# Kernel optimization log

Hardware: AMD Instinct MI355X
Metric: run time of the kernel (lower is better)

## Reference

```python
import jax, jax.numpy as jnp
import numpy as np

B, T, N_EMBD, N_HEAD = 2, 2048, 1024, 16
HEAD = N_EMBD // N_HEAD
WINDOW = 64


def setup_inputs() -> dict:
    key = jax.random.key(0)
    kq, kk, kv, kw = jax.random.split(key, 4)
    q = jax.random.normal(kq, (B, T, N_EMBD), dtype=jnp.float32)
    k = jax.random.normal(kk, (B, T, N_EMBD), dtype=jnp.float32)
    v = jax.random.normal(kv, (B, T, N_EMBD), dtype=jnp.float32)
    W_proj = jax.random.normal(kw, (N_EMBD, N_EMBD), dtype=jnp.float32) * (1.0 / np.sqrt(N_EMBD))
    b_proj = jnp.zeros((N_EMBD,), dtype=jnp.float32)
    return {"q": q, "k": k, "v": v, "W_proj": W_proj, "b_proj": b_proj}


def reference(q, k, v, W_proj, b_proj):
    Bsz, Tlen, _ = q.shape
    # split heads: [B, H, T, D]
    qh = q.reshape(Bsz, Tlen, N_HEAD, HEAD).transpose(0, 2, 1, 3)
    kh = k.reshape(Bsz, Tlen, N_HEAD, HEAD).transpose(0, 2, 1, 3)
    vh = v.reshape(Bsz, Tlen, N_HEAD, HEAD).transpose(0, 2, 1, 3)

    scale = 1.0 / np.sqrt(HEAD)
    scores = jnp.einsum('bhqd,bhkd->bhqk', qh, kh) * scale  # [B,H,T,T]

    # windowed additive mask: positions with |i-j| > WINDOW get -inf
    idx = jnp.arange(Tlen)
    dist = jnp.abs(idx[None, :] - idx[:, None])  # [T, T]
    scores = jnp.where(dist[None, None] > WINDOW, -jnp.inf, scores)

    attn = jax.nn.softmax(scores, axis=-1)
    y = jnp.einsum('bhqk,bhkd->bhqd', attn, vh)  # [B,H,T,D]
    y = y.transpose(0, 2, 1, 3).reshape(Bsz, Tlen, N_EMBD)
    return y @ W_proj.T + b_proj
```

## Files before the change

kernel.cpp:

```cpp
#include <hip/hip_runtime.h>
#include <hip/hip_bf16.h>

#define B_SZ 2
#define T_SZ 2048
#define NE   1024
#define NH   16
#define HD   64
#define WIN  64
#define QT   64
#define KT   192
#define GM   4096
#define GN   1024
#define GK   1024
#define KPAD 72
#define VPAD 200

__device__ ushort Wb_static[GN * GK];

__device__ __forceinline__ uint pack2(float lo, float hi) {
    uint r;
    asm("v_cvt_pk_bf16_f32 %0, %1, %2" : "=v"(r) : "v"(lo), "v"(hi));
    return r;
}
__device__ __forceinline__ uint4 pack8(float4 a, float4 b) {
    return make_uint4(pack2(a.x, a.y), pack2(a.z, a.w),
                      pack2(b.x, b.y), pack2(b.z, b.w));
}

typedef __attribute__((ext_vector_type(8))) short frag_ab;
typedef __attribute__((ext_vector_type(4))) float frag_cd;
union FragU { frag_ab f; uint u[4]; };

#define LDS_BAR() do {                                        \
    asm volatile("s_waitcnt lgkmcnt(0)" ::: "memory");        \
    __builtin_amdgcn_s_barrier();                             \
    asm volatile("" ::: "memory");                            \
} while (0)

#define VM_BAR(N) do {                                        \
    asm volatile("s_waitcnt vmcnt(" #N ")" ::: "memory");     \
    __builtin_amdgcn_s_barrier();                             \
    asm volatile("" ::: "memory");                            \
} while (0)

__global__ __launch_bounds__(256, 3) void attn_mfma_kernel(
    const float* __restrict__ q, const float* __restrict__ k,
    const float* __restrict__ v, const float* __restrict__ W,
    ushort* __restrict__ y)
{
    __shared__ __attribute__((aligned(16))) ushort pool[KT * KPAD + HD * VPAD];
    ushort* Ks = pool;
    ushort* Vt = pool + KT * KPAD;
    ushort* Ps = pool;

    const int bid = blockIdx.x;
    const int swz = ((bid & 7) << 7) | (bid >> 3);
    const int qs  = (swz & 31) * QT;
    const int h   = (swz >> 5) & 15;
    const int b   = swz >> 9;
    const int t   = threadIdx.x;
    const int kstart = qs - WIN;

    const int wv   = t >> 6;
    const int L    = t & 63;
    const int r16  = L & 15;
    const int quad = L >> 4;

    float4 qf0, qf1, qg0, qg1;
    {
        const float* qrow = q + ((size_t)(b * T_SZ + qs + wv * 16 + r16)) * NE + h * HD;
        const float4* p0 = (const float4*)(qrow + quad * 8);
        const float4* p1 = (const float4*)(qrow + 32 + quad * 8);
        qf0 = p0[0]; qf1 = p0[1]; qg0 = p1[0]; qg1 = p1[1];
    }

    {
        const int idx = bid * 256 + t;
        const float4 f = ((const float4*)W)[idx];
        ((uint2*)Wb_static)[idx] = make_uint2(pack2(f.x, f.y), pack2(f.z, f.w));
    }

    float4 va[6], vb[6];
#pragma unroll
    for (int i = 0; i < 6; ++i) {
        const int c  = t + 256 * i;
        const int j  = c >> 3;
        const int cc = c & 7;
        const int d8 = cc * 8;
        const int jg = kstart + j;
        const int jc = min(max(jg, 0), T_SZ - 1);
        const size_t off = ((size_t)(b * T_SZ + jc)) * NE + h * HD + d8;
        const float4* kp = (const float4*)(k + off);
        const float4* vp = (const float4*)(v + off);
        va[i] = vp[0]; vb[i] = vp[1];
        const float4 k0 = kp[0], k1 = kp[1];
        *(uint4*)&Ks[j * KPAD + d8] = pack8(k0, k1);
    }

    const float QSC = 0.125f * 1.44269504f;
    frag_ab aq0, aq1;
    {
        FragU u0, u1;
        u0.u[0] = pack2(qf0.x * QSC, qf0.y * QSC);
        u0.u[1] = pack2(qf0.z * QSC, qf0.w * QSC);
        u0.u[2] = pack2(qf1.x * QSC, qf1.y * QSC);
        u0.u[3] = pack2(qf1.z * QSC, qf1.w * QSC);
        u1.u[0] = pack2(qg0.x * QSC, qg0.y * QSC);
        u1.u[1] = pack2(qg0.z * QSC, qg0.w * QSC);
        u1.u[2] = pack2(qg1.x * QSC, qg1.y * QSC);
        u1.u[3] = pack2(qg1.z * QSC, qg1.w * QSC);
        aq0 = u0.f; aq1 = u1.f;
    }
    LDS_BAR();

    frag_cd sacc[9];
#pragma unroll
    for (int i = 0; i < 9; ++i) sacc[i] = (frag_cd){0,0,0,0};
    __builtin_amdgcn_s_setprio(1);
#pragma unroll
    for (int i = 0; i < 9; ++i) {
        const int nb = wv + i;
        const frag_ab b0 = *(const frag_ab*)&Ks[(nb * 16 + r16) * KPAD + quad * 8];
        const frag_ab b1 = *(const frag_ab*)&Ks[(nb * 16 + r16) * KPAD + 32 + quad * 8];
        sacc[i] = __builtin_amdgcn_mfma_f32_16x16x32_bf16(aq0, b0, sacc[i], 0, 0, 0);
        sacc[i] = __builtin_amdgcn_mfma_f32_16x16x32_bf16(aq1, b1, sacc[i], 0, 0, 0);
    }
    __builtin_amdgcn_s_setprio(0);

    const int base_m = wv * 16 + quad * 4;
    float l[4] = {0.f, 0.f, 0.f, 0.f};
#pragma unroll
    for (int i = 0; i < 9; ++i) {
        const int jl = (wv + i) * 16 + r16;
        const int jg = kstart + jl;
        const bool jg_ok = (jg >= 0) & (jg < T_SZ);
#pragma unroll
        for (int r = 0; r < 4; ++r) {
            const int mrow = base_m + r;
            const bool valid = jg_ok & ((uint)(jl - mrow) <= 2u * WIN);
            const float p = valid ? exp2f(sacc[i][r]) : 0.0f;
            l[r] += p;
            sacc[i][r] = p;
        }
    }
#pragma unroll
    for (int r = 0; r < 4; ++r) {
        l[r] += __shfl_xor(l[r], 1);
        l[r] += __shfl_xor(l[r], 2);
        l[r] += __shfl_xor(l[r], 4);
        l[r] += __shfl_xor(l[r], 8);
    }

#pragma unroll
    for (int i = 0; i < 6; ++i) {
        const int c  = t + 256 * i;
        const int j  = c >> 3;
        const int cc = c & 7;
        const int d8 = cc * 8;
        ushort* vtc = &Vt[d8 * VPAD + (((j >> 3) ^ cc) * 8 + (j & 7))];
        const uint p01 = pack2(va[i].x, va[i].y);
        const uint p23 = pack2(va[i].z, va[i].w);
        const uint p45 = pack2(vb[i].x, vb[i].y);
        const uint p67 = pack2(vb[i].z, vb[i].w);
        vtc[0 * VPAD] = (ushort)p01; vtc[1 * VPAD] = (ushort)(p01 >> 16);
        vtc[2 * VPAD] = (ushort)p23; vtc[3 * VPAD] = (ushort)(p23 >> 16);
        vtc[4 * VPAD] = (ushort)p45; vtc[5 * VPAD] = (ushort)(p45 >> 16);
        vtc[6 * VPAD] = (ushort)p67; vtc[7 * VPAD] = (ushort)(p67 >> 16);
    }

    LDS_BAR();
#pragma unroll
    for (int i = 0; i < 9; ++i) {
        const int jl = (wv + i) * 16 + r16;
        const uint p01 = pack2(sacc[i][0], sacc[i][1]);
        const uint p23 = pack2(sacc[i][2], sacc[i][3]);
        Ps[(base_m + 0) * VPAD + jl] = (ushort)p01;
        Ps[(base_m + 1) * VPAD + jl] = (ushort)(p01 >> 16);
        Ps[(base_m + 2) * VPAD + jl] = (ushort)p23;
        Ps[(base_m + 3) * VPAD + jl] = (ushort)(p23 >> 16);
    }
    {
        const int zb = (wv & 1) ? (wv - 1) : (wv + 9);
        const int jl = zb * 16 + r16;
#pragma unroll
        for (int r = 0; r < 4; ++r)
            Ps[(base_m + r) * VPAD + jl] = 0;
    }
    LDS_BAR();

    const int kb0 = wv >> 1;
    frag_ab ap[5];
#pragma unroll
    for (int i = 0; i < 5; ++i)
        ap[i] = *(const frag_ab*)&Ps[(wv * 16 + r16) * VPAD + (kb0 + i) * 32 + quad * 8];

    frag_cd oacc[4];
#pragma unroll
    for (int nb = 0; nb < 4; ++nb) oacc[nb] = (frag_cd){0,0,0,0};
    __builtin_amdgcn_s_setprio(1);
#pragma unroll
    for (int nb = 0; nb < 4; ++nb) {
        const int dr  = nb * 16 + r16;
        const int dsw = (dr >> 3) & 7;
#pragma unroll
        for (int i = 0; i < 5; ++i) {
            const int kb = kb0 + i;
            const frag_ab bv = *(const frag_ab*)&Vt[dr * VPAD + (((kb * 4 + quad) ^ dsw) * 8)];
            oacc[nb] = __builtin_amdgcn_mfma_f32_16x16x32_bf16(ap[i], bv, oacc[nb], 0, 0, 0);
        }
    }
    __builtin_amdgcn_s_setprio(0);

    float inv[4];
#pragma unroll
    for (int r = 0; r < 4; ++r) inv[r] = 1.0f / l[r];
#pragma unroll
    for (int nb = 0; nb < 4; ++nb) {
        const int d  = nb * 16 + r16;
        const uint p01 = pack2(oacc[nb][0] * inv[0], oacc[nb][1] * inv[1]);
        const uint p23 = pack2(oacc[nb][2] * inv[2], oacc[nb][3] * inv[3]);
        const size_t rb = (size_t)(b * T_SZ + qs + base_m) * NE + h * HD + d;
        y[rb + 0 * NE] = (ushort)p01;
        y[rb + 1 * NE] = (ushort)(p01 >> 16);
        y[rb + 2 * NE] = (ushort)p23;
        y[rb + 3 * NE] = (ushort)(p23 >> 16);
    }
}

#define ASZ (128 * 64)
#define BSZ (64 * 64)

__global__ __launch_bounds__(256, 2) void proj_gemm_kernel(
    const ushort* __restrict__ A,
    const float* __restrict__ bias, float* __restrict__ C)
{
    __shared__ __attribute__((aligned(16))) ushort As[2 * ASZ];
    __shared__ __attribute__((aligned(16))) ushort Bs[2 * BSZ];

    const ushort* Bw = Wb_static;
    const int t   = threadIdx.x;
    const int bid = blockIdx.x;
    const int swz = ((bid & 7) << 6) | (bid >> 3);
    const int tile_n = swz & 15;
    const int tile_m = swz >> 4;
    const int lane   = t & 63;
    const int wv     = t >> 6;
    const int wm     = wv >> 1;
    const int wn     = wv & 1;
    const int r16    = lane & 15;
    const int quad   = lane >> 4;

    frag_cd acc[4][2];
#pragma unroll
    for (int mi = 0; mi < 4; ++mi)
#pragma unroll
        for (int ni = 0; ni < 2; ++ni)
            acc[mi][ni] = (frag_cd){0.0f, 0.0f, 0.0f, 0.0f};

    const int fm = wm * 64 + r16;
    const int fn = wn * 32 + r16;
    const int sw = r16 & 7;

#define STAGE_AB(buf, kk)                                                      \
    {                                                                          \
        _Pragma("unroll")                                                      \
        for (int i = 0; i < 4; ++i) {                                          \
            const int c   = t + 256 * i;                                       \
            const int row = c >> 3;                                            \
            const int src = ((c & 7) ^ (row & 7)) * 8;                         \
            __builtin_amdgcn_global_load_lds(                                  \
                (const __attribute__((address_space(1))) unsigned int*)        \
                    (A + (size_t)(tile_m * 128 + row) * GK + (kk) + src),      \
                (__attribute__((address_space(3))) unsigned int*)              \
                    (As + (buf) * ASZ + c * 8), 16, 0, 0);                     \
        }                                                                      \
        _Pragma("unroll")                                                      \
        for (int i = 0; i < 2; ++i) {                                          \
            const int c   = t + 256 * i;                                       \
            const int row = c >> 3;                                            \
            const int src = ((c & 7) ^ (row & 7)) * 8;                         \
            __builtin_amdgcn_global_load_lds(                                  \
                (const __attribute__((address_space(1))) unsigned int*)        \
                    (Bw + (size_t)(tile_n * 64 + row) * GK + (kk) + src),      \
                (__attribute__((address_space(3))) unsigned int*)              \
                    (Bs + (buf) * BSZ + c * 8), 16, 0, 0);                     \
        }                                                                      \
    }

#define COMPUTE_AB(buf)                                                        \
    {                                                                          \
        _Pragma("unroll")                                                      \
        for (int ks = 0; ks < 2; ++ks) {                                       \
            const int cidx = (((ks * 4) + quad) ^ sw) * 8;                     \
            frag_ab af[4], bfr[2];                                             \
            _Pragma("unroll")                                                  \
            for (int mi = 0; mi < 4; ++mi)                                     \
                af[mi] = *(const frag_ab*)                                     \
                    &As[(buf) * ASZ + (fm + mi * 16) * 64 + cidx];             \
            _Pragma("unroll")                                                  \
            for (int ni = 0; ni < 2; ++ni)                                     \
                bfr[ni] = *(const frag_ab*)                                    \
                    &Bs[(buf) * BSZ + (fn + ni * 16) * 64 + cidx];             \
            _Pragma("unroll")                                                  \
            for (int mi = 0; mi < 4; ++mi)                                     \
                _Pragma("unroll")                                              \
                for (int ni = 0; ni < 2; ++ni)                                 \
                    acc[mi][ni] = __builtin_amdgcn_mfma_f32_16x16x32_bf16(     \
                        af[mi], bfr[ni], acc[mi][ni], 0, 0, 0);                \
        }                                                                      \
    }

    STAGE_AB(0, 0);
    int cur = 0;
    for (int k0 = 0; k0 < GK - 64; k0 += 64) {
        STAGE_AB(cur ^ 1, k0 + 64);
        VM_BAR(6);
        COMPUTE_AB(cur);
        LDS_BAR();
        cur ^= 1;
    }
    {
        asm volatile("s_waitcnt vmcnt(0)" ::: "memory");
        __builtin_amdgcn_s_barrier();
        asm volatile("" ::: "memory");
        COMPUTE_AB(cur);
    }

#pragma unroll
    for (int mi = 0; mi < 4; ++mi) {
#pragma unroll
        for (int ni = 0; ni < 2; ++ni) {
            const int rbase = tile_m * 128 + wm * 64 + mi * 16 + quad * 4;
            const int cg    = tile_n * 64 + wn * 32 + ni * 16 + r16;
            const float bv  = bias[cg];
#pragma unroll
            for (int r = 0; r < 4; ++r)
                C[(size_t)(rbase + r) * GN + cg] = acc[mi][ni][r] + bv;
        }
    }
}

extern "C" void kernel_launch(void* const* d_in, const int* in_sizes, int n_in,
                              void* d_out, int out_size, void* d_ws, size_t ws_size,
                              hipStream_t stream) {
    (void)in_sizes; (void)n_in; (void)out_size; (void)ws_size;
    const float* q    = (const float*)d_in[0];
    const float* k    = (const float*)d_in[1];
    const float* v    = (const float*)d_in[2];
    const float* W    = (const float*)d_in[3];
    const float* bias = (const float*)d_in[4];
    float*  out = (float*)d_out;
    ushort* y   = (ushort*)d_ws;

    dim3 g1(1024);
    attn_mfma_kernel<<<g1, 256, 0, stream>>>(q, k, v, W, y);

    dim3 g2(512);
    proj_gemm_kernel<<<g2, 256, 0, stream>>>(y, bias, out);
}
```

Baseline: 119.1 us.

## Fuse attention and projection GEMM into one persistent kernel with grid barrier

Merges the windowed-attention kernel and the output-projection GEMM into a single 512-block launch. Each block now handles two query tiles of attention in a loop, then waits on a software grid-wide barrier built from an atomic counter before running its GEMM tile. The shared-memory pool is reused for the GEMM staging buffers. This removes the second kernel launch and the gap between kernels. In exchange, the attention phase runs with fewer blocks and lower occupancy, and correctness depends on all 512 blocks being resident at once for the spin barrier.

```diff
diff --git a/kernel.cpp b/kernel.cpp
--- a/kernel.cpp
+++ b/kernel.cpp
@@ -16,6 +16,7 @@
 #define VPAD 200
 
 __device__ ushort Wb_static[GN * GK];
+__device__ unsigned long long bar_count = 0;
 
 __device__ __forceinline__ uint pack2(float lo, float hi) {
     uint r;
@@ -43,9 +44,13 @@
     asm volatile("" ::: "memory");                            \
 } while (0)
 
-__global__ __launch_bounds__(256, 3) void attn_mfma_kernel(
+#define ASZ (128 * 64)
+#define BSZ (64 * 64)
+
+__global__ __launch_bounds__(256, 2) void fused_kernel(
     const float* __restrict__ q, const float* __restrict__ k,
     const float* __restrict__ v, const float* __restrict__ W,
+    const float* __restrict__ bias, float* __restrict__ out,
     ushort* __restrict__ y)
 {
     __shared__ __attribute__((aligned(16))) ushort pool[KT * KPAD + HD * VPAD];
@@ -54,212 +59,214 @@
     ushort* Ps = pool;
 
     const int bid = blockIdx.x;
-    const int swz = ((bid & 7) << 7) | (bid >> 3);
-    const int qs  = (swz & 31) * QT;
-    const int h   = (swz >> 5) & 15;
-    const int b   = swz >> 9;
+    const int s   = ((bid & 7) << 6) | (bid >> 3);
+    const int h   = (s >> 4) & 15;
+    const int b   = s >> 8;
     const int t   = threadIdx.x;
-    const int kstart = qs - WIN;
 
     const int wv   = t >> 6;
     const int L    = t & 63;
     const int r16  = L & 15;
     const int quad = L >> 4;
 
-    float4 qf0, qf1, qg0, qg1;
+    for (int rep = 0; rep < 2; ++rep) {
+        LDS_BAR();
+
+        const int qs = ((s & 15) * 2 + rep) * QT;
+        const int kstart = qs - WIN;
+
+        float4 qf0, qf1, qg0, qg1;
+        {
+            const float* qrow = q + ((size_t)(b * T_SZ + qs + wv * 16 + r16)) * NE + h * HD;
+            const float4* p0 = (const float4*)(qrow + quad * 8);
+            const float4* p1 = (const float4*)(qrow + 32 + quad * 8);
+            qf0 = p0[0]; qf1 = p0[1]; qg0 = p1[0]; qg1 = p1[1];
+        }
+
+        {
+            const int idx = (bid * 2 + rep) * 256 + t;
+            const float4 f = ((const float4*)W)[idx];
+            ((uint2*)Wb_static)[idx] = make_uint2(pack2(f.x, f.y), pack2(f.z, f.w));
+        }
+
+        float4 va[6], vb[6];
+#pragma unroll
+        for (int i = 0; i < 6; ++i) {
+            const int c  = t + 256 * i;
+            const int j  = c >> 3;
+            const int cc = c & 7;
+            const int d8 = cc * 8;
+            const int jg = kstart + j;
+            const int jc = min(max(jg, 0), T_SZ - 1);
+            const size_t off = ((size_t)(b * T_SZ + jc)) * NE + h * HD + d8;
+            const float4* kp = (const float4*)(k + off);
+            const float4* vp = (const float4*)(v + off);
+            va[i] = vp[0]; vb[i] = vp[1];
+            const float4 k0 = kp[0], k1 = kp[1];
+            *(uint4*)&Ks[j * KPAD + d8] = pack8(k0, k1);
+        }
+
+        const float QSC = 0.125f * 1.44269504f;
+        frag_ab aq0, aq1;
+        {
+            FragU u0, u1;
+            u0.u[0] = pack2(qf0.x * QSC, qf0.y * QSC);
+            u0.u[1] = pack2(qf0.z * QSC, qf0.w * QSC);
+            u0.u[2] = pack2(qf1.x * QSC, qf1.y * QSC);
+            u0.u[3] = pack2(qf1.z * QSC, qf1.w * QSC);
+            u1.u[0] = pack2(qg0.x * QSC, qg0.y * QSC);
+            u1.u[1] = pack2(qg0.z * QSC, qg0.w * QSC);
+            u1.u[2] = pack2(qg1.x * QSC, qg1.y * QSC);
+            u1.u[3] = pack2(qg1.z * QSC, qg1.w * QSC);
+            aq0 = u0.f; aq1 = u1.f;
+        }
+        LDS_BAR();
+
+        frag_cd sacc[9];
+#pragma unroll
+        for (int i = 0; i < 9; ++i) sacc[i] = (frag_cd){0,0,0,0};
+        __builtin_amdgcn_s_setprio(1);
+#pragma unroll
+        for (int i = 0; i < 9; ++i) {
+            const int nb = wv + i;
+            const frag_ab b0 = *(const frag_ab*)&Ks[(nb * 16 + r16) * KPAD + quad * 8];
+            const frag_ab b1 = *(const frag_ab*)&Ks[(nb * 16 + r16) * KPAD + 32 + quad * 8];
+            sacc[i] = __builtin_amdgcn_mfma_f32_16x16x32_bf16(aq0, b0, sacc[i], 0, 0, 0);
+            sacc[i] = __builtin_amdgcn_mfma_f32_16x16x32_bf16(aq1, b1, sacc[i], 0, 0, 0);
+        }
+        __builtin_amdgcn_s_setprio(0);
+
+        const int base_m = wv * 16 + quad * 4;
+        float l[4] = {0.f, 0.f, 0.f, 0.f};
+#pragma unroll
+        for (int i = 0; i < 9; ++i) {
+            const int jl = (wv + i) * 16 + r16;
+            const int jg = kstart + jl;
+            const bool jg_ok = (jg >= 0) & (jg < T_SZ);
+#pragma unroll
+            for (int r = 0; r < 4; ++r) {
+                const int mrow = base_m + r;
+                const bool valid = jg_ok & ((uint)(jl - mrow) <= 2u * WIN);
+                const float p = valid ? exp2f(sacc[i][r]) : 0.0f;
+                l[r] += p;
+                sacc[i][r] = p;
+            }
+        }
+#pragma unroll
+        for (int r = 0; r < 4; ++r) {
+            l[r] += __shfl_xor(l[r], 1);
+            l[r] += __shfl_xor(l[r], 2);
+            l[r] += __shfl_xor(l[r], 4);
+            l[r] += __shfl_xor(l[r], 8);
+        }
+
+#pragma unroll
+        for (int i = 0; i < 6; ++i) {
+            const int c  = t + 256 * i;
+            const int j  = c >> 3;
+            const int cc = c & 7;
+            const int d8 = cc * 8;
+            ushort* vtc = &Vt[d8 * VPAD + (((j >> 3) ^ cc) * 8 + (j & 7))];
+            const uint p01 = pack2(va[i].x, va[i].y);
+            const uint p23 = pack2(va[i].z, va[i].w);
+            const uint p45 = pack2(vb[i].x, vb[i].y);
+            const uint p67 = pack2(vb[i].z, vb[i].w);
+            vtc[0 * VPAD] = (ushort)p01; vtc[1 * VPAD] = (ushort)(p01 >> 16);
+            vtc[2 * VPAD] = (ushort)p23; vtc[3 * VPAD] = (ushort)(p23 >> 16);
+            vtc[4 * VPAD] = (ushort)p45; vtc[5 * VPAD] = (ushort)(p45 >> 16);
+            vtc[6 * VPAD] = (ushort)p67; vtc[7 * VPAD] = (ushort)(p67 >> 16);
+        }
+
+        LDS_BAR();
+#pragma unroll
+        for (int i = 0; i < 9; ++i) {
+            const int jl = (wv + i) * 16 + r16;
+            const uint p01 = pack2(sacc[i][0], sacc[i][1]);
+            const uint p23 = pack2(sacc[i][2], sacc[i][3]);
+            Ps[(base_m + 0) * VPAD + jl] = (ushort)p01;
+            Ps[(base_m + 1) * VPAD + jl] = (ushort)(p01 >> 16);
+            Ps[(base_m + 2) * VPAD + jl] = (ushort)p23;
+            Ps[(base_m + 3) * VPAD + jl] = (ushort)(p23 >> 16);
+        }
+        {
+            const int zb = (wv & 1) ? (wv - 1) : (wv + 9);
+            const int jl = zb * 16 + r16;
+#pragma unroll
+            for (int r = 0; r < 4; ++r)
+                Ps[(base_m + r) * VPAD + jl] = 0;
+        }
+        LDS_BAR();
+
+        const int kb0 = wv >> 1;
+        frag_ab ap[5];
+#pragma unroll
+        for (int i = 0; i < 5; ++i)
+            ap[i] = *(const frag_ab*)&Ps[(wv * 16 + r16) * VPAD + (kb0 + i) * 32 + quad * 8];
+
+        frag_cd oacc[4];
+#pragma unroll
+        for (int nb = 0; nb < 4; ++nb) oacc[nb] = (frag_cd){0,0,0,0};
+        __builtin_amdgcn_s_setprio(1);
+#pragma unroll
+        for (int nb = 0; nb < 4; ++nb) {
+            const int dr  = nb * 16 + r16;
+            const int dsw = (dr >> 3) & 7;
+#pragma unroll
+            for (int i = 0; i < 5; ++i) {
+                const int kb = kb0 + i;
+                const frag_ab bv = *(const frag_ab*)&Vt[dr * VPAD + (((kb * 4 + quad) ^ dsw) * 8)];
+                oacc[nb] = __builtin_amdgcn_mfma_f32_16x16x32_bf16(ap[i], bv, oacc[nb], 0, 0, 0);
+            }
+        }
+        __builtin_amdgcn_s_setprio(0);
+
+        float inv[4];
+#pragma unroll
+        for (int r = 0; r < 4; ++r) inv[r] = 1.0f / l[r];
+#pragma unroll
+        for (int nb = 0; nb < 4; ++nb) {
+            const int d  = nb * 16 + r16;
+            const uint p01 = pack2(oacc[nb][0] * inv[0], oacc[nb][1] * inv[1]);
+            const uint p23 = pack2(oacc[nb][2] * inv[2], oacc[nb][3] * inv[3]);
+            const size_t rb = (size_t)(b * T_SZ + qs + base_m) * NE + h * HD + d;
+            y[rb + 0 * NE] = (ushort)p01;
+            y[rb + 1 * NE] = (ushort)(p01 >> 16);
+            y[rb + 2 * NE] = (ushort)p23;
+            y[rb + 3 * NE] = (ushort)(p23 >> 16);
+        }
+    }
+
+    __syncthreads();
+    __threadfence();
+    if (t == 0) {
+        const unsigned long long my = atomicAdd(&bar_count, 1ULL) + 1ULL;
+        const unsigned long long target = ((my + 511ULL) / 512ULL) * 512ULL;
+        while (atomicAdd(&bar_count, 0ULL) < target)
+            __builtin_amdgcn_s_sleep(2);
+    }
+    __syncthreads();
+    __threadfence();
+
     {
-        const float* qrow = q + ((size_t)(b * T_SZ + qs + wv * 16 + r16)) * NE + h * HD;
-        const float4* p0 = (const float4*)(qrow + quad * 8);
-        const float4* p1 = (const float4*)(qrow + 32 + quad * 8);
-        qf0 = p0[0]; qf1 = p0[1]; qg0 = p1[0]; qg1 = p1[1];
-    }
-
-    {
-        const int idx = bid * 256 + t;
-        const float4 f = ((const float4*)W)[idx];
-        ((uint2*)Wb_static)[idx] = make_uint2(pack2(f.x, f.y), pack2(f.z, f.w));
-    }
-
-    float4 va[6], vb[6];
-#pragma unroll
-    for (int i = 0; i < 6; ++i) {
-        const int c  = t + 256 * i;
-        const int j  = c >> 3;
-        const int cc = c & 7;
-        const int d8 = cc * 8;
-        const int jg = kstart + j;
-        const int jc = min(max(jg, 0), T_SZ - 1);
-        const size_t off = ((size_t)(b * T_SZ + jc)) * NE + h * HD + d8;
-        const float4* kp = (const float4*)(k + off);
-        const float4* vp = (const float4*)(v + off);
-        va[i] = vp[0]; vb[i] = vp[1];
-        const float4 k0 = kp[0], k1 = kp[1];
-        *(uint4*)&Ks[j * KPAD + d8] = pack8(k0, k1);
-    }
-
-    const float QSC = 0.125f * 1.44269504f;
-    frag_ab aq0, aq1;
-    {
-        FragU u0, u1;
-        u0.u[0] = pack2(qf0.x * QSC, qf0.y * QSC);
-        u0.u[1] = pack2(qf0.z * QSC, qf0.w * QSC);
-        u0.u[2] = pack2(qf1.x * QSC, qf1.y * QSC);
-        u0.u[3] = pack2(qf1.z * QSC, qf1.w * QSC);
-        u1.u[0] = pack2(qg0.x * QSC, qg0.y * QSC);
-        u1.u[1] = pack2(qg0.z * QSC, qg0.w * QSC);
-        u1.u[2] = pack2(qg1.x * QSC, qg1.y * QSC);
-        u1.u[3] = pack2(qg1.z * QSC, qg1.w * QSC);
-        aq0 = u0.f; aq1 = u1.f;
-    }
-    LDS_BAR();
-
-    frag_cd sacc[9];
-#pragma unroll
-    for (int i = 0; i < 9; ++i) sacc[i] = (frag_cd){0,0,0,0};
-    __builtin_amdgcn_s_setprio(1);
-#pragma unroll
-    for (int i = 0; i < 9; ++i) {
-        const int nb = wv + i;
-        const frag_ab b0 = *(const frag_ab*)&Ks[(nb * 16 + r16) * KPAD + quad * 8];
-        const frag_ab b1 = *(const frag_ab*)&Ks[(nb * 16 + r16) * KPAD + 32 + quad * 8];
-        sacc[i] = __builtin_amdgcn_mfma_f32_16x16x32_bf16(aq0, b0, sacc[i], 0, 0, 0);
-        sacc[i] = __builtin_amdgcn_mfma_f32_16x16x32_bf16(aq1, b1, sacc[i], 0, 0, 0);
-    }
-    __builtin_amdgcn_s_setprio(0);
-
-    const int base_m = wv * 16 + quad * 4;
-    float l[4] = {0.f, 0.f, 0.f, 0.f};
-#pragma unroll
-    for (int i = 0; i < 9; ++i) {
-        const int jl = (wv + i) * 16 + r16;
-        const int jg = kstart + jl;
-        const bool jg_ok = (jg >= 0) & (jg < T_SZ);
-#pragma unroll
-        for (int r = 0; r < 4; ++r) {
-            const int mrow = base_m + r;
-            const bool valid = jg_ok & ((uint)(jl - mrow) <= 2u * WIN);
-            const float p = valid ? exp2f(sacc[i][r]) : 0.0f;
-            l[r] += p;
-            sacc[i][r] = p;
-        }
-    }
-#pragma unroll
-    for (int r = 0; r < 4; ++r) {
-        l[r] += __shfl_xor(l[r], 1);
-        l[r] += __shfl_xor(l[r], 2);
-        l[r] += __shfl_xor(l[r], 4);
-        l[r] += __shfl_xor(l[r], 8);
-    }
-
-#pragma unroll
-    for (int i = 0; i < 6; ++i) {
-        const int c  = t + 256 * i;
-        const int j  = c >> 3;
-        const int cc = c & 7;
-        const int d8 = cc * 8;
-        ushort* vtc = &Vt[d8 * VPAD + (((j >> 3) ^ cc) * 8 + (j & 7))];
-        const uint p01 = pack2(va[i].x, va[i].y);
-        const uint p23 = pack2(va[i].z, va[i].w);
-        const uint p45 = pack2(vb[i].x, vb[i].y);
-        const uint p67 = pack2(vb[i].z, vb[i].w);
-        vtc[0 * VPAD] = (ushort)p01; vtc[1 * VPAD] = (ushort)(p01 >> 16);
-        vtc[2 * VPAD] = (ushort)p23; vtc[3 * VPAD] = (ushort)(p23 >> 16);
-        vtc[4 * VPAD] = (ushort)p45; vtc[5 * VPAD] = (ushort)(p45 >> 16);
-        vtc[6 * VPAD] = (ushort)p67; vtc[7 * VPAD] = (ushort)(p67 >> 16);
-    }
-
-    LDS_BAR();
-#pragma unroll
-    for (int i = 0; i < 9; ++i) {
-        const int jl = (wv + i) * 16 + r16;
-        const uint p01 = pack2(sacc[i][0], sacc[i][1]);
-        const uint p23 = pack2(sacc[i][2], sacc[i][3]);
-        Ps[(base_m + 0) * VPAD + jl] = (ushort)p01;
-        Ps[(base_m + 1) * VPAD + jl] = (ushort)(p01 >> 16);
-        Ps[(base_m + 2) * VPAD + jl] = (ushort)p23;
-        Ps[(base_m + 3) * VPAD + jl] = (ushort)(p23 >> 16);
-    }
-    {
-        const int zb = (wv & 1) ? (wv - 1) : (wv + 9);
-        const int jl = zb * 16 + r16;
-#pragma unroll
-        for (int r = 0; r < 4; ++r)
-            Ps[(base_m + r) * VPAD + jl] = 0;
-    }
-    LDS_BAR();
-
-    const int kb0 = wv >> 1;
-    frag_ab ap[5];
-#pragma unroll
-    for (int i = 0; i < 5; ++i)
-        ap[i] = *(const frag_ab*)&Ps[(wv * 16 + r16) * VPAD + (kb0 + i) * 32 + quad * 8];
-
-    frag_cd oacc[4];
-#pragma unroll
-    for (int nb = 0; nb < 4; ++nb) oacc[nb] = (frag_cd){0,0,0,0};
-    __builtin_amdgcn_s_setprio(1);
-#pragma unroll
-    for (int nb = 0; nb < 4; ++nb) {
-        const int dr  = nb * 16 + r16;
-        const int dsw = (dr >> 3) & 7;
-#pragma unroll
-        for (int i = 0; i < 5; ++i) {
-            const int kb = kb0 + i;
-            const frag_ab bv = *(const frag_ab*)&Vt[dr * VPAD + (((kb * 4 + quad) ^ dsw) * 8)];
-            oacc[nb] = __builtin_amdgcn_mfma_f32_16x16x32_bf16(ap[i], bv, oacc[nb], 0, 0, 0);
-        }
-    }
-    __builtin_amdgcn_s_setprio(0);
-
-    float inv[4];
-#pragma unroll
-    for (int r = 0; r < 4; ++r) inv[r] = 1.0f / l[r];
-#pragma unroll
-    for (int nb = 0; nb < 4; ++nb) {
-        const int d  = nb * 16 + r16;
-        const uint p01 = pack2(oacc[nb][0] * inv[0], oacc[nb][1] * inv[1]);
-        const uint p23 = pack2(oacc[nb][2] * inv[2], oacc[nb][3] * inv[3]);
-        const size_t rb = (size_t)(b * T_SZ + qs + base_m) * NE + h * HD + d;
-        y[rb + 0 * NE] = (ushort)p01;
-        y[rb + 1 * NE] = (ushort)(p01 >> 16);
-        y[rb + 2 * NE] = (ushort)p23;
-        y[rb + 3 * NE] = (ushort)(p23 >> 16);
-    }
-}
-
-#define ASZ (128 * 64)
-#define BSZ (64 * 64)
-
-__global__ __launch_bounds__(256, 2) void proj_gemm_kernel(
-    const ushort* __restrict__ A,
-    const float* __restrict__ bias, float* __restrict__ C)
-{
-    __shared__ __attribute__((aligned(16))) ushort As[2 * ASZ];
-    __shared__ __attribute__((aligned(16))) ushort Bs[2 * BSZ];
-
-    const ushort* Bw = Wb_static;
-    const int t   = threadIdx.x;
-    const int bid = blockIdx.x;
-    const int swz = ((bid & 7) << 6) | (bid >> 3);
-    const int tile_n = swz & 15;
-    const int tile_m = swz >> 4;
-    const int lane   = t & 63;
-    const int wv     = t >> 6;
-    const int wm     = wv >> 1;
-    const int wn     = wv & 1;
-    const int r16    = lane & 15;
-    const int quad   = lane >> 4;
-
-    frag_cd acc[4][2];
-#pragma unroll
-    for (int mi = 0; mi < 4; ++mi)
-#pragma unroll
-        for (int ni = 0; ni < 2; ++ni)
-            acc[mi][ni] = (frag_cd){0.0f, 0.0f, 0.0f, 0.0f};
-
-    const int fm = wm * 64 + r16;
-    const int fn = wn * 32 + r16;
-    const int sw = r16 & 7;
+        ushort* As = pool;
+        ushort* Bs = pool + 2 * ASZ;
+
+        const ushort* Bw = Wb_static;
+        const int tile_n = s & 15;
+        const int tile_m = s >> 4;
+        const int wm = wv >> 1;
+        const int wn = wv & 1;
+
+        frag_cd acc[4][2];
+#pragma unroll
+        for (int mi = 0; mi < 4; ++mi)
+#pragma unroll
+            for (int ni = 0; ni < 2; ++ni)
+                acc[mi][ni] = (frag_cd){0.0f, 0.0f, 0.0f, 0.0f};
+
+        const int fm = wm * 64 + r16;
+        const int fn = wn * 32 + r16;
+        const int sw = r16 & 7;
 
 #define STAGE_AB(buf, kk)                                                      \
     {                                                                          \
@@ -270,7 +277,7 @@
             const int src = ((c & 7) ^ (row & 7)) * 8;                         \
             __builtin_amdgcn_global_load_lds(                                  \
                 (const __attribute__((address_space(1))) unsigned int*)        \
-                    (A + (size_t)(tile_m * 128 + row) * GK + (kk) + src),      \
+                    (y + (size_t)(tile_m * 128 + row) * GK + (kk) + src),      \
                 (__attribute__((address_space(3))) unsigned int*)              \
                     (As + (buf) * ASZ + c * 8), 16, 0, 0);                     \
         }                                                                      \
@@ -310,32 +317,33 @@
         }                                                                      \
     }
 
-    STAGE_AB(0, 0);
-    int cur = 0;
-    for (int k0 = 0; k0 < GK - 64; k0 += 64) {
-        STAGE_AB(cur ^ 1, k0 + 64);
-        VM_BAR(6);
-        COMPUTE_AB(cur);
-        LDS_BAR();
-        cur ^= 1;
-    }
-    {
-        asm volatile("s_waitcnt vmcnt(0)" ::: "memory");
-        __builtin_amdgcn_s_barrier();
-        asm volatile("" ::: "memory");
-        COMPUTE_AB(cur);
-    }
-
-#pragma unroll
-    for (int mi = 0; mi < 4; ++mi) {
-#pragma unroll
-        for (int ni = 0; ni < 2; ++ni) {
-            const int rbase = tile_m * 128 + wm * 64 + mi * 16 + quad * 4;
-            const int cg    = tile_n * 64 + wn * 32 + ni * 16 + r16;
-            const float bv  = bias[cg];
-#pragma unroll
-            for (int r = 0; r < 4; ++r)
-                C[(size_t)(rbase + r) * GN + cg] = acc[mi][ni][r] + bv;
+        STAGE_AB(0, 0);
+        int cur = 0;
+        for (int k0 = 0; k0 < GK - 64; k0 += 64) {
+            STAGE_AB(cur ^ 1, k0 + 64);
+            VM_BAR(6);
+            COMPUTE_AB(cur);
+            LDS_BAR();
+            cur ^= 1;
+        }
+        {
+            asm volatile("s_waitcnt vmcnt(0)" ::: "memory");
+            __builtin_amdgcn_s_barrier();
+            asm volatile("" ::: "memory");
+            COMPUTE_AB(cur);
+        }
+
+#pragma unroll
+        for (int mi = 0; mi < 4; ++mi) {
+#pragma unroll
+            for (int ni = 0; ni < 2; ++ni) {
+                const int rbase = tile_m * 128 + wm * 64 + mi * 16 + quad * 4;
+                const int cg    = tile_n * 64 + wn * 32 + ni * 16 + r16;
+                const float bv  = bias[cg];
+#pragma unroll
+                for (int r = 0; r < 4; ++r)
+                    out[(size_t)(rbase + r) * GN + cg] = acc[mi][ni][r] + bv;
+            }
         }
     }
 }
@@ -352,9 +360,5 @@
     float*  out = (float*)d_out;
     ushort* y   = (ushort*)d_ws;
 
-    dim3 g1(1024);
-    attn_mfma_kernel<<<g1, 256, 0, stream>>>(q, k, v, W, y);
-
-    dim3 g2(512);
-    proj_gemm_kernel<<<g2, 256, 0, stream>>>(y, bias, out);
+    fused_kernel<<<dim3(512), 256, 0, stream>>>(q, k, v, W, bias, out, y);
 }
```

New measurement: 233.5 us. 96.1% more time.
